# Performance work log

Hardware: AMD Instinct MI355X
Metric: run time of the kernel (lower is better)

## Reference

```python
import jax, jax.numpy as jnp
import numpy as np

B, H, W, DIM, NH, WS, SS = 32, 56, 56, 512, 16, 7, 3
L = H * W
HD = DIM // NH
N = WS * WS
SCALE = HD ** -0.5
EPS = 1e-5


def _rel_pos_index():
    coords = np.stack(np.meshgrid(np.arange(WS), np.arange(WS), indexing='ij'))  # (2,ws,ws)
    cf = coords.reshape(2, -1)
    rc = (cf[:, :, None] - cf[:, None, :]).transpose(1, 2, 0).astype(np.int64)  # (N,N,2)
    rc[..., 0] += WS - 1
    rc[..., 1] += WS - 1
    rc[..., 0] *= 2 * WS - 1
    return rc.sum(-1)  # (N,N)


def _shift_mask():
    img = np.zeros((H, W), np.float32)
    cnt = 0
    for hs in (slice(0, -WS), slice(-WS, -SS), slice(-SS, None)):
        for ws_ in (slice(0, -WS), slice(-WS, -SS), slice(-SS, None)):
            img[hs, ws_] = cnt
            cnt += 1
    m = img.reshape(H // WS, WS, W // WS, WS).transpose(0, 2, 1, 3).reshape(-1, N)  # (nW,N)
    diff = m[:, None, :] - m[:, :, None]
    return np.where(diff != 0, -100.0, 0.0).astype(np.float32)  # (nW,N,N)


REL_IDX = jnp.asarray(_rel_pos_index())
ATTN_MASK = jnp.asarray(_shift_mask())


def _ln(x, g, b):
    mu = jnp.mean(x, -1, keepdims=True)
    var = jnp.var(x, -1, keepdims=True)
    return (x - mu) * jax.lax.rsqrt(var + EPS) * g + b


def setup_inputs() -> dict:
    key = jax.random.key(0)
    ks = jax.random.split(key, 8)
    s = 0.02
    return {
        'x': jax.random.normal(ks[0], (B, L, DIM), jnp.float32),
        'norm1_g': jnp.ones((DIM,), jnp.float32),
        'norm1_b': jnp.zeros((DIM,), jnp.float32),
        'qkv_w': jax.random.normal(ks[1], (DIM, 3 * DIM), jnp.float32) * s,
        'qkv_b': jnp.zeros((3 * DIM,), jnp.float32),
        'rel_bias_table': jax.random.normal(ks[2], ((2 * WS - 1) ** 2, NH), jnp.float32) * s,
        'proj_w': jax.random.normal(ks[3], (DIM, DIM), jnp.float32) * s,
        'proj_b': jnp.zeros((DIM,), jnp.float32),
        'norm2_g': jnp.ones((DIM,), jnp.float32),
        'norm2_b': jnp.zeros((DIM,), jnp.float32),
        'fc1_w': jax.random.normal(ks[4], (DIM, 4 * DIM), jnp.float32) * s,
        'fc1_b': jnp.zeros((4 * DIM,), jnp.float32),
        'fc2_w': jax.random.normal(ks[5], (4 * DIM, DIM), jnp.float32) * s,
        'fc2_b': jnp.zeros((DIM,), jnp.float32),
    }


def reference(x, norm1_g, norm1_b, qkv_w, qkv_b, rel_bias_table, proj_w, proj_b,
              norm2_g, norm2_b, fc1_w, fc1_b, fc2_w, fc2_b):
    shortcut = x
    h = _ln(x, norm1_g, norm1_b).reshape(B, H, W, DIM)
    # cyclic shift
    h = jnp.roll(h, (-SS, -SS), axis=(1, 2))
    # window partition -> (B*nW, N, C)
    nWh, nWw = H // WS, W // WS
    h = h.reshape(B, nWh, WS, nWw, WS, DIM).transpose(0, 1, 3, 2, 4, 5).reshape(-1, N, DIM)
    Bw = h.shape[0]
    # qkv
    qkv = (h @ qkv_w + qkv_b).reshape(Bw, N, 3, NH, HD).transpose(2, 0, 3, 1, 4)
    q, k, v = qkv[0], qkv[1], qkv[2]  # (Bw, NH, N, HD)
    attn = jnp.einsum('bhnd,bhmd->bhnm', q * SCALE, k)
    # relative position bias (NH, N, N)
    bias = rel_bias_table[REL_IDX.reshape(-1)].reshape(N, N, NH).transpose(2, 0, 1)
    attn = attn + bias[None]
    # shift mask: (B, nW, NH, N, N) + (1, nW, 1, N, N)
    nW = nWh * nWw
    attn = attn.reshape(B, nW, NH, N, N) + ATTN_MASK[None, :, None]
    attn = jax.nn.softmax(attn.reshape(Bw, NH, N, N), axis=-1)
    out = jnp.einsum('bhnm,bhmd->bhnd', attn, v).transpose(0, 2, 1, 3).reshape(Bw, N, DIM)
    out = out @ proj_w + proj_b
    # window reverse + reverse shift
    out = out.reshape(B, nWh, nWw, WS, WS, DIM).transpose(0, 1, 3, 2, 4, 5).reshape(B, H, W, DIM)
    out = jnp.roll(out, (SS, SS), axis=(1, 2)).reshape(B, L, DIM)
    x = shortcut + out
    # MLP (GELU exact, matching torch nn.GELU default)
    y = _ln(x, norm2_g, norm2_b)
    y = jax.nn.gelu(y @ fc1_w + fc1_b, approximate=False) @ fc2_w + fc2_b
    return x + y
```

## Files before the change

### kernel.cpp

```cpp
#include <hip/hip_runtime.h>
#include <hip/hip_bf16.h>
#include <math.h>

#define MROWS 100352
#define MHALF 50176
#define DIM   512
#define LL    3136
#define HH    56
#define SSH   3
#define SCALE_QK 0.17677669529663687f

typedef __bf16 bf16;
typedef __bf16 bf16x8 __attribute__((ext_vector_type(8)));
typedef float  f32x4  __attribute__((ext_vector_type(4)));

typedef __attribute__((address_space(1))) void* gas_ptr;
typedef __attribute__((address_space(3))) void* las_ptr;

__device__ __forceinline__ void gload_lds16(const void* g, void* l) {
  __builtin_amdgcn_global_load_lds((gas_ptr)g, (las_ptr)l, 16, 0, 0);
}

__device__ __forceinline__ int nat_row(int r) {
  int bw = r / 49;
  int n  = r - bw * 49;
  int b  = bw >> 6;
  int wh = (bw >> 3) & 7;
  int ww = bw & 7;
  int i  = n / 7;
  int j  = n - i * 7;
  int hs = wh * 7 + i + SSH; if (hs >= HH) hs -= HH;
  int ws = ww * 7 + j + SSH; if (ws >= HH) ws -= HH;
  return b * LL + hs * HH + ws;
}

__global__ __launch_bounds__(256) void tcast_kernel(const float* __restrict__ src,
                                                    bf16* __restrict__ dst,
                                                    int Kd, int Nd) {
  __shared__ float t[32][33];
  int tx = threadIdx.x & 31, ty = threadIdx.x >> 5;
  int n0 = blockIdx.x * 32, k0 = blockIdx.y * 32;
  #pragma unroll
  for (int yy = ty; yy < 32; yy += 8)
    t[yy][tx] = src[(size_t)(k0 + yy) * Nd + n0 + tx];
  __syncthreads();
  #pragma unroll
  for (int yy = ty; yy < 32; yy += 8)
    dst[(size_t)(n0 + yy) * Kd + k0 + tx] = (bf16)t[tx][yy];
}

__global__ __launch_bounds__(256) void biasM_kernel(const float* __restrict__ table,
                                                    float* __restrict__ biasM) {
  int e = blockIdx.x * 256 + threadIdx.x;
  if (e >= 4 * 16 * 2401) return;
  int k  = e % 49;
  int t  = e / 49;
  int qv = t % 49; t /= 49;
  int head = t & 15;
  int cls  = t >> 4;
  int i1 = qv / 7, j1 = qv - i1 * 7;
  int i2 = k / 7,  j2 = k - i2 * 7;
  float b = table[((i1 - i2 + 6) * 13 + (j1 - j2 + 6)) * 16 + head];
  int labq = ((cls & 2) ? ((i1 < 4) ? 1 : 2) : 0) * 3 + ((cls & 1) ? ((j1 < 4) ? 1 : 2) : 0);
  int labk = ((cls & 2) ? ((i2 < 4) ? 1 : 2) : 0) * 3 + ((cls & 1) ? ((j2 < 4) ? 1 : 2) : 0);
  biasM[e] = b + ((labq == labk) ? 0.f : -100.f);
}

template<int PERM>
__global__ __launch_bounds__(256) void ln_kernel(const float* __restrict__ x,
                                                 const float* __restrict__ gw,
                                                 const float* __restrict__ bw_,
                                                 bf16* __restrict__ out) {
  int wave = threadIdx.x >> 6, lane = threadIdx.x & 63;
  int r = blockIdx.x * 4 + wave;
  int src = PERM ? nat_row(r) : r;
  const float* px = x + (size_t)src * DIM + lane * 8;
  float4 v0 = *(const float4*)px;
  float4 v1 = *(const float4*)(px + 4);
  float s = v0.x + v0.y + v0.z + v0.w + v1.x + v1.y + v1.z + v1.w;
  float q = v0.x*v0.x + v0.y*v0.y + v0.z*v0.z + v0.w*v0.w
          + v1.x*v1.x + v1.y*v1.y + v1.z*v1.z + v1.w*v1.w;
  #pragma unroll
  for (int m = 1; m < 64; m <<= 1) { s += __shfl_xor(s, m); q += __shfl_xor(q, m); }
  float mean = s * (1.f / DIM);
  float var  = q * (1.f / DIM) - mean * mean;
  float rstd = rsqrtf(var + 1e-5f);
  int c0 = lane * 8;
  float4 g0 = *(const float4*)(gw + c0),  g1 = *(const float4*)(gw + c0 + 4);
  float4 b0 = *(const float4*)(bw_ + c0), b1 = *(const float4*)(bw_ + c0 + 4);
  bf16x8 o;
  o[0] = (bf16)((v0.x - mean) * rstd * g0.x + b0.x);
  o[1] = (bf16)((v0.y - mean) * rstd * g0.y + b0.y);
  o[2] = (bf16)((v0.z - mean) * rstd * g0.z + b0.z);
  o[3] = (bf16)((v0.w - mean) * rstd * g0.w + b0.w);
  o[4] = (bf16)((v1.x - mean) * rstd * g1.x + b1.x);
  o[5] = (bf16)((v1.y - mean) * rstd * g1.y + b1.y);
  o[6] = (bf16)((v1.z - mean) * rstd * g1.z + b1.z);
  o[7] = (bf16)((v1.w - mean) * rstd * g1.w + b1.w);
  *(bf16x8*)(out + (size_t)r * DIM + c0) = o;
}


#define MF(a,b,c) __builtin_amdgcn_mfma_f32_16x16x32_bf16((a),(b),(c),0,0,0)
#define BAR() __builtin_amdgcn_s_barrier()
#define WLG() asm volatile("s_waitcnt lgkmcnt(0)" ::: "memory")
#define WVM(n) asm volatile("s_waitcnt vmcnt(" #n ")" ::: "memory")

template<int MODE, int KD, int ND>
__global__ __launch_bounds__(512, 2) void gemm256_kernel(const bf16* __restrict__ A,
                                                         const bf16* __restrict__ Bt,
                                                         const float* __restrict__ bias,
                                                         const float* __restrict__ resid,
                                                         bf16* __restrict__ outB,
                                                         float* __restrict__ outF,
                                                         bf16* __restrict__ outK,
                                                         bf16* __restrict__ outV) {
  constexpr int NTN = ND / 256;
  constexpr int NI  = KD / 128;
  __shared__ bf16 lds[65536];

  const int tid = threadIdx.x, lane = tid & 63, wv = tid >> 6;
  const int lr = lane & 15, lg = lane >> 4;
  const int wm = wv >> 2, wn = wv & 3;

  int nwg = gridDim.x, orig = blockIdx.x;
  int q = nwg >> 3, r = nwg & 7, xcd = orig & 7;
  int wgid = (xcd < r ? xcd * (q + 1) : r * (q + 1) + (xcd - r) * q) + (orig >> 3);
  int tm = wgid / NTN, tn = wgid % NTN;

  const bf16* gA = A  + (size_t)tm * 256 * KD;
  const bf16* gB = Bt + (size_t)tn * 256 * KD;

  const int klg  = (lg * 8) ^ ((lr & 8) ? 16 : 0);
  const int a_rd = (wm * 128 + lr) * 32 + klg;
  const int b_rd = (wn * 64 + lr) * 32 + klg;

  const int kbOffE = (wv >> 2) * 8192;
  const int kGlob  = (wv >> 2) * 32 + (((lane & 3) * 8) ^ ((lane & 32) ? 16 : 0));
  const int rl0    = ((wv * 2) & 7) * 16 + (lane >> 2);
  const int rl1    = rl0 + 16;
  const int c0off  = ((wv * 2) & 7) * 512;

#define STG(GP, DB, h, koff) \
  gload_lds16((GP) + (size_t)((h) * 128 + rl0) * KD + (koff) + kGlob, \
              (void*)(lds + (DB) + kbOffE + (h) * 4096 + c0off)); \
  gload_lds16((GP) + (size_t)((h) * 128 + rl1) * KD + (koff) + kGlob, \
              (void*)(lds + (DB) + kbOffE + (h) * 4096 + c0off + 512));

  f32x4 acc[8][4];
  #pragma unroll
  for (int i = 0; i < 8; i++)
    #pragma unroll
    for (int j = 0; j < 4; j++) { acc[i][j][0]=0.f; acc[i][j][1]=0.f; acc[i][j][2]=0.f; acc[i][j][3]=0.f; }

  bf16x8 Af[4][2], Bf0[2][2], Bf1[2][2];

  STG(gA, 0,     0, 0)  STG(gA, 0,     1, 0)
  STG(gB, 16384, 0, 0)  STG(gB, 16384, 1, 0)
  STG(gA, 32768, 0, 64) STG(gA, 32768, 1, 64)
  STG(gB, 49152, 0, 64) STG(gB, 49152, 1, 64)
  WVM(8); BAR();

#define PHASES(AB, BB, DOST, KST, ENDW) { \
    _Pragma("unroll") for (int m = 0; m < 4; m++) { \
      Af[m][0] = *(const bf16x8*)(lds + (AB) + m * 512 + a_rd); \
      Af[m][1] = *(const bf16x8*)(lds + (AB) + 8192 + m * 512 + a_rd); } \
    _Pragma("unroll") for (int n = 0; n < 2; n++) { \
      Bf0[n][0] = *(const bf16x8*)(lds + (BB) + n * 512 + b_rd); \
      Bf0[n][1] = *(const bf16x8*)(lds + (BB) + 8192 + n * 512 + b_rd); } \
    BAR(); WLG(); __builtin_amdgcn_s_setprio(1); \
    _Pragma("unroll") for (int m = 0; m < 4; m++) \
      _Pragma("unroll") for (int n = 0; n < 2; n++) { \
        acc[m][n] = MF(Af[m][0], Bf0[n][0], acc[m][n]); \
        acc[m][n] = MF(Af[m][1], Bf0[n][1], acc[m][n]); } \
    __builtin_amdgcn_s_setprio(0); BAR(); \
    _Pragma("unroll") for (int n = 0; n < 2; n++) { \
      Bf1[n][0] = *(const bf16x8*)(lds + (BB) + (n + 2) * 512 + b_rd); \
      Bf1[n][1] = *(const bf16x8*)(lds + (BB) + 8192 + (n + 2) * 512 + b_rd); } \
    if (DOST) { STG(gB, (BB), 0, (KST)) } \
    BAR(); WLG(); __builtin_amdgcn_s_setprio(1); \
    _Pragma("unroll") for (int m = 0; m < 4; m++) \
      _Pragma("unroll") for (int n = 0; n < 2; n++) { \
        acc[m][n + 2] = MF(Af[m][0], Bf1[n][0], acc[m][n + 2]); \
        acc[m][n + 2] = MF(Af[m][1], Bf1[n][1], acc[m][n + 2]); } \
    __builtin_amdgcn_s_setprio(0); BAR(); \
    _Pragma("unroll") for (int m = 0; m < 4; m++) { \
      Af[m][0] = *(const bf16x8*)(lds + (AB) + (m + 4) * 512 + a_rd); \
      Af[m][1] = *(const bf16x8*)(lds + (AB) + 8192 + (m + 4) * 512 + a_rd); } \
    if (DOST) { STG(gB, (BB), 1, (KST)) STG(gA, (AB), 0, (KST)) } \
    BAR(); WLG(); __builtin_amdgcn_s_setprio(1); \
    _Pragma("unroll") for (int m = 0; m < 4; m++) \
      _Pragma("unroll") for (int n = 0; n < 2; n++) { \
        acc[m + 4][n + 2] = MF(Af[m][0], Bf1[n][0], acc[m + 4][n + 2]); \
        acc[m + 4][n + 2] = MF(Af[m][1], Bf1[n][1], acc[m + 4][n + 2]); } \
    __builtin_amdgcn_s_setprio(0); BAR(); \
    if (DOST) { STG(gA, (AB), 1, (KST)) } \
    BAR(); WLG(); __builtin_amdgcn_s_setprio(1); \
    _Pragma("unroll") for (int m = 0; m < 4; m++) \
      _Pragma("unroll") for (int n = 0; n < 2; n++) { \
        acc[m + 4][n] = MF(Af[m][0], Bf0[n][0], acc[m + 4][n]); \
        acc[m + 4][n] = MF(Af[m][1], Bf0[n][1], acc[m + 4][n]); } \
    __builtin_amdgcn_s_setprio(0); ENDW; BAR(); \
  }

  #pragma unroll 1
  for (int I = 0; I < NI - 1; ++I) {
    int ke = (2 * I + 2) * 64;
    PHASES(0,     16384, 1, ke,      WVM(6));
    PHASES(32768, 49152, 1, ke + 64, WVM(6));
  }
  PHASES(0,     16384, 0, 0, WVM(0));
  PHASES(32768, 49152, 0, 0, ((void)0));

#undef PHASES
#undef STG

  #pragma unroll
  for (int fm = 0; fm < 8; fm++) {
    #pragma unroll
    for (int rr = 0; rr < 4; rr++) {
      int row = tm * 256 + wm * 128 + fm * 16 + lg * 4 + rr;
      int orow = (MODE == 1) ? nat_row(row) : row;
      int win = 0, nn = 0;
      if (MODE == 4) { win = row / 49; nn = row - win * 49; }
      #pragma unroll
      for (int fn = 0; fn < 4; fn++) {
        int col = tn * 256 + wn * 64 + fn * 16 + lr;
        float v = acc[fm][fn][rr] + bias[col];
        if (MODE == 1) {
          outF[(size_t)orow * ND + col] = resid[(size_t)orow * ND + col] + v;
        } else if (MODE == 2) {
          float g = 0.5f * v * (1.f + erff(v * 0.70710678118654752f));
          outB[(size_t)row * ND + col] = (bf16)g;
        } else if (MODE == 3) {
          outF[(size_t)row * ND + col] = resid[(size_t)row * ND + col] + v;
        } else if (MODE == 4) {
          int c = col & 511;
          int head = c >> 5, d = c & 31;
          size_t sb = (size_t)(win * 16 + head);
          if (col < 512)        outB[sb * 1568 + nn * 32 + d] = (bf16)v;
          else if (col < 1024)  outK[sb * 1568 + nn * 32 + d] = (bf16)v;
          else                  outV[sb * 2048 + d * 64 + nn] = (bf16)v;
        }
      }
    }
  }
}

__global__ __launch_bounds__(256) void attn_kernel(const bf16* __restrict__ Qb,
                                                   const bf16* __restrict__ Kb,
                                                   const bf16* __restrict__ Vt,
                                                   const float* __restrict__ biasM,
                                                   bf16* __restrict__ attnO) {
  __shared__ bf16 P[4][64 * 72];
  int wave = threadIdx.x >> 6, lane = threadIdx.x & 63;
  int lr = lane & 15, lg = lane >> 4;
  int wid = blockIdx.x * 4 + wave;
  int win = wid >> 4, head = wid & 15;
  int wh = (win >> 3) & 7, ww = win & 7;
  int cls = ((wh == 7) ? 2 : 0) | ((ww == 7) ? 1 : 0);
  const bf16* qp = Qb + (size_t)wid * 1568;
  const bf16* kp = Kb + (size_t)wid * 1568;
  const bf16* vp = Vt + (size_t)wid * 2048;
  const float* bp = biasM + (size_t)cls * 38416 + head * 2401;

  f32x4 zero4 = {0.f, 0.f, 0.f, 0.f};
  bf16x8 aq[4], bk[4];
  #pragma unroll
  for (int mi = 0; mi < 4; mi++) {
    int qq = mi * 16 + lr; if (qq > 48) qq = 48;
    aq[mi] = *(const bf16x8*)(qp + qq * 32 + lg * 8);
    bk[mi] = *(const bf16x8*)(kp + qq * 32 + lg * 8);
  }
  f32x4 sacc[4][4];
  #pragma unroll
  for (int mi = 0; mi < 4; mi++)
    #pragma unroll
    for (int ni = 0; ni < 4; ni++)
      sacc[mi][ni] = __builtin_amdgcn_mfma_f32_16x16x32_bf16(aq[mi], bk[ni], zero4, 0, 0, 0);

  float rsum[4][4];
  #pragma unroll
  for (int mi = 0; mi < 4; mi++) {
    #pragma unroll
    for (int rr = 0; rr < 4; rr++) {
      int qrow = mi * 16 + lg * 4 + rr;
      int qc = qrow > 48 ? 48 : qrow;
      const float* bq = bp + qc * 49;
      float pv[4];
      float mv = -3.0e30f;
      #pragma unroll
      for (int ni = 0; ni < 4; ni++) {
        int key = ni * 16 + lr;
        float v = (key < 49) ? sacc[mi][ni][rr] * SCALE_QK + bq[key] : -1e30f;
        pv[ni] = v;
        mv = fmaxf(mv, v);
      }
      #pragma unroll
      for (int m = 1; m < 16; m <<= 1) mv = fmaxf(mv, __shfl_xor(mv, m));
      float sum = 0.f;
      #pragma unroll
      for (int ni = 0; ni < 4; ni++) {
        float p = __expf(pv[ni] - mv);
        sum += p;
        P[wave][qrow * 72 + ni * 16 + lr] = (bf16)p;
      }
      #pragma unroll
      for (int m = 1; m < 16; m <<= 1) sum += __shfl_xor(sum, m);
      rsum[mi][rr] = sum;
    }
  }
  __syncthreads();

  f32x4 oacc[4][2];
  #pragma unroll
  for (int mi = 0; mi < 4; mi++) { oacc[mi][0] = zero4; oacc[mi][1] = zero4; }
  #pragma unroll
  for (int ks = 0; ks < 2; ks++) {
    bf16x8 bv[2];
    #pragma unroll
    for (int n2 = 0; n2 < 2; n2++)
      bv[n2] = *(const bf16x8*)(vp + (n2 * 16 + lr) * 64 + ks * 32 + lg * 8);
    #pragma unroll
    for (int mi = 0; mi < 4; mi++) {
      bf16x8 ap = *(const bf16x8*)(&P[wave][(mi * 16 + lr) * 72 + ks * 32 + lg * 8]);
      #pragma unroll
      for (int n2 = 0; n2 < 2; n2++)
        oacc[mi][n2] = __builtin_amdgcn_mfma_f32_16x16x32_bf16(ap, bv[n2], oacc[mi][n2], 0, 0, 0);
    }
  }
  #pragma unroll
  for (int mi = 0; mi < 4; mi++) {
    #pragma unroll
    for (int rr = 0; rr < 4; rr++) {
      int qrow = mi * 16 + lg * 4 + rr;
      if (qrow < 49) {
        float inv = 1.f / rsum[mi][rr];
        #pragma unroll
        for (int n2 = 0; n2 < 2; n2++)
          attnO[((size_t)win * 49 + qrow) * DIM + head * 32 + n2 * 16 + lr] =
              (bf16)(oacc[mi][n2][rr] * inv);
      }
    }
  }
}

extern "C" void kernel_launch(void* const* d_in, const int* in_sizes, int n_in,
                              void* d_out, int out_size, void* d_ws, size_t ws_size,
                              hipStream_t stream) {
  const float* x      = (const float*)d_in[0];
  const float* n1g    = (const float*)d_in[1];
  const float* n1b    = (const float*)d_in[2];
  const float* qkv_w  = (const float*)d_in[3];
  const float* qkv_b  = (const float*)d_in[4];
  const float* tabl   = (const float*)d_in[5];
  const float* proj_w = (const float*)d_in[6];
  const float* proj_b = (const float*)d_in[7];
  const float* n2g    = (const float*)d_in[8];
  const float* n2b    = (const float*)d_in[9];
  const float* fc1_w  = (const float*)d_in[10];
  const float* fc1_b  = (const float*)d_in[11];
  const float* fc2_w  = (const float*)d_in[12];
  const float* fc2_b  = (const float*)d_in[13];
  float* out = (float*)d_out;

  char* ws = (char*)d_ws;
  bf16*  RegA   = (bf16*)ws;
  bf16*  Qb     = (bf16*)(ws + 102760448);
  bf16*  Kb     = (bf16*)(ws + 102760448 + 102760448);
  bf16*  RegB   = Qb;
  char*  reg2   = ws + 411041792;
  bf16*  Vt     = (bf16*)reg2;
  float* biasM  = (float*)(reg2 + 134217728);
  float* x2     = (float*)reg2;
  bf16*  qkvWt  = (bf16*)(ws + 616562688);
  bf16*  projWt = qkvWt + 1536 * 512;
  bf16*  fc1Wt  = projWt + 512 * 512;
  bf16*  fc2Wt  = fc1Wt + 2048 * 512;

  biasM_kernel<<<(4 * 16 * 2401 + 255) / 256, 256, 0, stream>>>(tabl, biasM);
  tcast_kernel<<<dim3(1536 / 32, 512 / 32), 256, 0, stream>>>(qkv_w, qkvWt, 512, 1536);
  tcast_kernel<<<dim3(512 / 32, 512 / 32), 256, 0, stream>>>(proj_w, projWt, 512, 512);
  tcast_kernel<<<dim3(2048 / 32, 512 / 32), 256, 0, stream>>>(fc1_w, fc1Wt, 512, 2048);
  tcast_kernel<<<dim3(512 / 32, 2048 / 32), 256, 0, stream>>>(fc2_w, fc2Wt, 2048, 512);

  ln_kernel<1><<<MROWS / 4, 256, 0, stream>>>(x, n1g, n1b, RegA);
  gemm256_kernel<4, 512, 1536><<<(MROWS / 256) * 6, 512, 0, stream>>>(
      RegA, qkvWt, qkv_b, nullptr, Qb, nullptr, Kb, Vt);
  attn_kernel<<<2048 * 16 / 4, 256, 0, stream>>>(Qb, Kb, Vt, biasM, RegA);
  gemm256_kernel<1, 512, 512><<<(MROWS / 256) * 2, 512, 0, stream>>>(
      RegA, projWt, proj_b, x, nullptr, x2, nullptr, nullptr);
  ln_kernel<0><<<MROWS / 4, 256, 0, stream>>>(x2, n2g, n2b, RegA);
  for (int c = 0; c < 2; ++c) {
    const bf16* a1 = RegA + (size_t)c * MHALF * 512;
    gemm256_kernel<2, 512, 2048><<<(MHALF / 256) * 8, 512, 0, stream>>>(
        a1, fc1Wt, fc1_b, nullptr, RegB, nullptr, nullptr, nullptr);
    gemm256_kernel<3, 2048, 512><<<(MHALF / 256) * 2, 512, 0, stream>>>(
        RegB, fc2Wt, fc2_b, x2 + (size_t)c * MHALF * 512, nullptr,
        out + (size_t)c * MHALF * 512, nullptr, nullptr);
  }
}
```

Before: 1.755 ms.

## Store V in natural layout and transpose through LDS inside attention

```diff
diff --git a/kernel.cpp b/kernel.cpp
--- a/kernel.cpp
+++ b/kernel.cpp
@@ -12,6 +12,7 @@
 
 typedef __bf16 bf16;
 typedef __bf16 bf16x8 __attribute__((ext_vector_type(8)));
+typedef __bf16 bf16x4 __attribute__((ext_vector_type(4)));
 typedef float  f32x4  __attribute__((ext_vector_type(4)));
 
 typedef __attribute__((address_space(1))) void* gas_ptr;
@@ -237,10 +238,10 @@
         } else if (MODE == 4) {
           int c = col & 511;
           int head = c >> 5, d = c & 31;
-          size_t sb = (size_t)(win * 16 + head);
-          if (col < 512)        outB[sb * 1568 + nn * 32 + d] = (bf16)v;
-          else if (col < 1024)  outK[sb * 1568 + nn * 32 + d] = (bf16)v;
-          else                  outV[sb * 2048 + d * 64 + nn] = (bf16)v;
+          size_t sb = (size_t)(win * 16 + head) * 1568 + nn * 32 + d;
+          if (col < 512)        outB[sb] = (bf16)v;
+          else if (col < 1024)  outK[sb] = (bf16)v;
+          else                  outV[sb] = (bf16)v;
         }
       }
     }
@@ -249,10 +250,11 @@
 
 __global__ __launch_bounds__(256) void attn_kernel(const bf16* __restrict__ Qb,
                                                    const bf16* __restrict__ Kb,
-                                                   const bf16* __restrict__ Vt,
+                                                   const bf16* __restrict__ Vb,
                                                    const float* __restrict__ biasM,
                                                    bf16* __restrict__ attnO) {
   __shared__ bf16 P[4][64 * 72];
+  __shared__ bf16 Vs[4][49 * 36];
   int wave = threadIdx.x >> 6, lane = threadIdx.x & 63;
   int lr = lane & 15, lg = lane >> 4;
   int wid = blockIdx.x * 4 + wave;
@@ -261,8 +263,15 @@
   int cls = ((wh == 7) ? 2 : 0) | ((ww == 7) ? 1 : 0);
   const bf16* qp = Qb + (size_t)wid * 1568;
   const bf16* kp = Kb + (size_t)wid * 1568;
-  const bf16* vp = Vt + (size_t)wid * 2048;
+  const bf16* vp = Vb + (size_t)wid * 1568;
   const float* bp = biasM + (size_t)cls * 38416 + head * 2401;
+
+  for (int i = lane; i < 196; i += 64) {
+    bf16x8 v = *(const bf16x8*)(vp + i * 8);
+    int nn = i >> 2, d = (i & 3) * 8;
+    ((bf16x4*)(&Vs[wave][nn * 36 + d]))[0] = ((bf16x4*)&v)[0];
+    ((bf16x4*)(&Vs[wave][nn * 36 + d + 4]))[0] = ((bf16x4*)&v)[1];
+  }
 
   f32x4 zero4 = {0.f, 0.f, 0.f, 0.f};
   bf16x8 aq[4], bk[4];
@@ -320,7 +329,12 @@
     bf16x8 bv[2];
     #pragma unroll
     for (int n2 = 0; n2 < 2; n2++)
-      bv[n2] = *(const bf16x8*)(vp + (n2 * 16 + lr) * 64 + ks * 32 + lg * 8);
+      #pragma unroll
+      for (int j = 0; j < 8; j++) {
+        int kv = ks * 32 + lg * 8 + j;
+        if (kv > 48) kv = 48;
+        bv[n2][j] = Vs[wave][kv * 36 + n2 * 16 + lr];
+      }
     #pragma unroll
     for (int mi = 0; mi < 4; mi++) {
       bf16x8 ap = *(const bf16x8*)(&P[wave][(mi * 16 + lr) * 72 + ks * 32 + lg * 8]);
@@ -369,11 +383,11 @@
   bf16*  Qb     = (bf16*)(ws + 102760448);
   bf16*  Kb     = (bf16*)(ws + 102760448 + 102760448);
   bf16*  RegB   = Qb;
-  char*  reg2   = ws + 411041792;
-  bf16*  Vt     = (bf16*)reg2;
-  float* biasM  = (float*)(reg2 + 134217728);
+  char*  reg2   = ws + 308281344;
+  bf16*  Vb     = (bf16*)reg2;
+  float* biasM  = (float*)(reg2 + 102760448);
   float* x2     = (float*)reg2;
-  bf16*  qkvWt  = (bf16*)(ws + 616562688);
+  bf16*  qkvWt  = (bf16*)(ws + 308281344 + 205520896);
   bf16*  projWt = qkvWt + 1536 * 512;
   bf16*  fc1Wt  = projWt + 512 * 512;
   bf16*  fc2Wt  = fc1Wt + 2048 * 512;
@@ -386,8 +400,8 @@
 
   ln_kernel<1><<<MROWS / 4, 256, 0, stream>>>(x, n1g, n1b, RegA);
   gemm256_kernel<4, 512, 1536><<<(MROWS / 256) * 6, 512, 0, stream>>>(
-      RegA, qkvWt, qkv_b, nullptr, Qb, nullptr, Kb, Vt);
-  attn_kernel<<<2048 * 16 / 4, 256, 0, stream>>>(Qb, Kb, Vt, biasM, RegA);
+      RegA, qkvWt, qkv_b, nullptr, Qb, nullptr, Kb, Vb);
+  attn_kernel<<<2048 * 16 / 4, 256, 0, stream>>>(Qb, Kb, Vb, biasM, RegA);
   gemm256_kernel<1, 512, 512><<<(MROWS / 256) * 2, 512, 0, stream>>>(
       RegA, projWt, proj_b, x, nullptr, x2, nullptr, nullptr);
   ln_kernel<0><<<MROWS / 4, 256, 0, stream>>>(x2, n2g, n2b, RegA);
```

Result: no change. 1.744 ms (-0.6%).
